# Kernel tuning notes

Measured on AMD Instinct MI355X. Metric: run time of the kernel, lower is better.

## Reference

```python
import jax, jax.numpy as jnp
import numpy as np

B, P, H, A = 256, 196, 1024, 512

def setup_inputs() -> dict:
    key = jax.random.key(0)
    ks = jax.random.split(key, 20)
    s = 1.0 / np.sqrt(H)
    sa = 1.0 / np.sqrt(A)
    return {
        "spatial_image": jax.random.normal(ks[0], (B, P, H), jnp.float32),
        "decoder_out": jax.random.normal(ks[1], (B, H), jnp.float32),
        "st": jax.random.normal(ks[2], (B, H), jnp.float32),
        "W_sen_aff": jax.random.uniform(ks[3], (H, H), jnp.float32, -s, s),
        "b_sen_aff": jax.random.uniform(ks[4], (H,), jnp.float32, -s, s),
        "W_sen_att": jax.random.uniform(ks[5], (H, A), jnp.float32, -s, s),
        "b_sen_att": jax.random.uniform(ks[6], (A,), jnp.float32, -s, s),
        "W_h_aff": jax.random.uniform(ks[7], (H, H), jnp.float32, -s, s),
        "b_h_aff": jax.random.uniform(ks[8], (H,), jnp.float32, -s, s),
        "W_h_att": jax.random.uniform(ks[9], (H, A), jnp.float32, -s, s),
        "b_h_att": jax.random.uniform(ks[10], (A,), jnp.float32, -s, s),
        "W_v_att": jax.random.uniform(ks[11], (H, A), jnp.float32, -s, s),
        "b_v_att": jax.random.uniform(ks[12], (A,), jnp.float32, -s, s),
        "W_alpha": jax.random.uniform(ks[13], (A, 1), jnp.float32, -sa, sa),
        "b_alpha": jax.random.uniform(ks[14], (1,), jnp.float32, -sa, sa),
        "W_ctx": jax.random.uniform(ks[15], (H, H), jnp.float32, -s, s),
        "b_ctx": jax.random.uniform(ks[16], (H,), jnp.float32, -s, s),
    }

def reference(spatial_image, decoder_out, st,
              W_sen_aff, b_sen_aff, W_sen_att, b_sen_att,
              W_h_aff, b_h_aff, W_h_att, b_h_att,
              W_v_att, b_v_att, W_alpha, b_alpha, W_ctx, b_ctx):
    # visual_attn: [B, P, A]
    visual_attn = jnp.einsum('bph,ha->bpa', spatial_image, W_v_att) + b_v_att
    # sentinel path: [B, H] -> relu affine -> [B, A]
    sentinel_affine = jax.nn.relu(st @ W_sen_aff + b_sen_aff)
    sentinel_attn = sentinel_affine @ W_sen_att + b_sen_att
    # hidden path: [B, H] -> tanh affine -> [B, A]
    hidden_affine = jnp.tanh(decoder_out @ W_h_aff + b_h_aff)
    hidden_attn = hidden_affine @ W_h_att + b_h_att
    # concat sentinel as an extra "pixel": [B, P+1, H] and [B, P+1, A]
    concat_features = jnp.concatenate([spatial_image, sentinel_affine[:, None, :]], axis=1)
    attended_features = jnp.concatenate([visual_attn, sentinel_attn[:, None, :]], axis=1)
    attention = jnp.tanh(attended_features + hidden_attn[:, None, :])  # [B, P+1, A]
    alpha = (jnp.einsum('bpa,ao->bpo', attention, W_alpha) + b_alpha)[..., 0]  # [B, P+1]
    att_weights = jax.nn.softmax(alpha, axis=1)
    context = jnp.einsum('bph,bp->bh', concat_features, att_weights)  # [B, H]
    beta_value = att_weights[:, -1:]  # [B, 1]
    out_l = jnp.tanh((context + hidden_affine) @ W_ctx + b_ctx)  # [B, H]
    return (out_l, att_weights, beta_value)
```

## Files before the change

### kernel.cpp

```cpp
#include <hip/hip_runtime.h>
#include <hip/hip_bf16.h>
#include <stdint.h>
#include <stddef.h>

typedef __attribute__((ext_vector_type(4))) float f32x4;
typedef __attribute__((ext_vector_type(8))) short short8;

#define MROWS 50176


static __device__ __forceinline__ int lds_off(int row, int k) {
    int slot = (k >> 3) ^ ((row >> 1) & 3);
    return (row << 6) + (slot << 4) + ((k & 7) << 1);
}

static __device__ __forceinline__ unsigned div196(unsigned g) {
    return (unsigned)(((unsigned long long)g * 85599ull) >> 24);
}

static __device__ __forceinline__ unsigned short f2bf(float f) {
    union { float f; unsigned u; } v; v.f = f;
    unsigned r = v.u + 0x7FFFu + ((v.u >> 16) & 1u);
    return (unsigned short)(r >> 16);
}

static __device__ __forceinline__ unsigned pack2bf(float2 a) {
    union { unsigned u; __hip_bfloat162 h; } r;
    r.h = __float22bfloat162_rn(a);
    return r.u;
}

static __device__ __forceinline__ unsigned long long pack4bf(f32x4 a) {
    union { unsigned long long u; __hip_bfloat162 h[2]; } r;
    r.h[0] = __float22bfloat162_rn(make_float2(a[0], a[1]));
    r.h[1] = __float22bfloat162_rn(make_float2(a[2], a[3]));
    return r.u;
}

static __device__ __forceinline__ float tanh_fast(float x) {
    float xc = fminf(fmaxf(x, -9.f), 9.f);
    float e = __builtin_amdgcn_exp2f(xc * 2.885390081777927f);
    return (e - 1.f) * __builtin_amdgcn_rcpf(e + 1.f);
}

static __device__ __forceinline__ void gload_lds16(const void* g, void* l) {
    __builtin_amdgcn_global_load_lds(
        (const __attribute__((address_space(1))) unsigned int*)g,
        (__attribute__((address_space(3))) unsigned int*)l, 16, 0, 0);
}

__global__ __launch_bounds__(512, 4) void attn_alpha_kernel(
    const float* __restrict__ spatial,
    const unsigned short* __restrict__ WvT,
    const float* __restrict__ b_v_att,
    const float* __restrict__ hidden_attn,
    const float* __restrict__ W_alpha,
    float* __restrict__ alphab)
{
    __shared__ char sA[2][2048];
    __shared__ char sB[32768];
    float* alpha_s = (float*)&sA[0][0];
    const int tid = threadIdx.x;
    const int row0 = blockIdx.x << 5;

    const int lane = tid & 63, w = tid >> 6;
    const int lrow = lane & 15, lk = lane >> 4;

    const int arow = tid >> 4;
    const int acol = (tid & 15) << 1;
    const float* Ap = spatial + (size_t)(row0 + arow) * 1024 + acol;
    const int aoff = lds_off(arow, acol);

    const unsigned short* Bq[4];
    int boff[4];
    #pragma unroll
    for (int c = 0; c < 4; ++c) {
        int row = (c << 7) + (w << 4) + (lane >> 2);
        int ke = (lane & 3) << 3;
        Bq[c] = WvT + (size_t)row * 1024 + ke;
        boff[c] = lds_off(row, ke);
    }

    f32x4 acc[2][4];
    f32x4 z = {0.f, 0.f, 0.f, 0.f};
    #pragma unroll
    for (int m = 0; m < 2; ++m)
        #pragma unroll
        for (int n = 0; n < 4; ++n) acc[m][n] = z;

    {
        float2 a0 = *(const float2*)Ap;
        f32x4 b0[4];
        #pragma unroll
        for (int c = 0; c < 4; ++c) b0[c] = *(const f32x4*)Bq[c];
        *(unsigned*)(sA[0] + aoff) = pack2bf(a0);
        #pragma unroll
        for (int c = 0; c < 4; ++c) *(f32x4*)(sB + boff[c]) = b0[c];
    }
    __syncthreads();

    for (int ks = 0; ks < 32; ++ks) {
        const int cur = ks & 1, nxt = cur ^ 1;
        float2 aN;
        f32x4 bN[4];
        if (ks < 31) {
            const int ko = (ks + 1) << 5;
            aN = *(const float2*)(Ap + ko);
            #pragma unroll
            for (int c = 0; c < 4; ++c) bN[c] = *(const f32x4*)(Bq[c] + ko);
        }
        short8 af[2], bf[4];
        #pragma unroll
        for (int m = 0; m < 2; ++m)
            af[m] = *(const short8*)(sA[cur] + lds_off((m << 4) + lrow, lk << 3));
        #pragma unroll
        for (int n = 0; n < 4; ++n)
            bf[n] = *(const short8*)(sB + lds_off((w << 6) + (n << 4) + lrow, lk << 3));
        #pragma unroll
        for (int m = 0; m < 2; ++m)
            #pragma unroll
            for (int n = 0; n < 4; ++n)
                acc[m][n] = __builtin_amdgcn_mfma_f32_16x16x32_bf16(af[m], bf[n], acc[m][n], 0, 0, 0);
        __syncthreads();
        if (ks < 31) {
            *(unsigned*)(sA[nxt] + aoff) = pack2bf(aN);
            #pragma unroll
            for (int c = 0; c < 4; ++c) *(f32x4*)(sB + boff[c]) = bN[c];
            __syncthreads();
        }
    }

    if (tid < 32) alpha_s[tid] = 0.f;
    __syncthreads();

    const unsigned bb0 = div196((unsigned)row0);
    const unsigned bb1 = div196((unsigned)(row0 + 31));
    float bv[4], wa[4], h0[4], h1[4];
    #pragma unroll
    for (int n = 0; n < 4; ++n) {
        int g = (w << 6) + (n << 4) + lrow;
        bv[n] = b_v_att[g];
        wa[n] = W_alpha[g];
        h0[n] = hidden_attn[bb0 * 512 + g];
        h1[n] = hidden_attn[bb1 * 512 + g];
    }
    #pragma unroll
    for (int m = 0; m < 2; ++m) {
        #pragma unroll
        for (int i = 0; i < 4; ++i) {
            int rloc = (m << 4) + (lk << 2) + i;
            bool first = (div196((unsigned)(row0 + rloc)) == bb0);
            float s = 0.f;
            #pragma unroll
            for (int n = 0; n < 4; ++n) {
                float v = tanh_fast(acc[m][n][i] + bv[n] + (first ? h0[n] : h1[n]));
                s += v * wa[n];
            }
            #pragma unroll
            for (int off = 1; off < 16; off <<= 1) s += __shfl_xor(s, off);
            if (lrow == 0) atomicAdd(&alpha_s[rloc], s);
        }
    }
    __syncthreads();
    if (tid < 32) {
        unsigned g = (unsigned)(row0 + tid);
        unsigned bb = div196(g);
        unsigned p = g - bb * 196;
        alphab[bb * 196 + p] = alpha_s[tid];
    }
}

static __device__ __forceinline__ void kloop_dbuf(
    const float* __restrict__ Abase,
    const unsigned short* __restrict__ Bbase,
    char* sA0, char* sA1, char* sB0, char* sB1,
    f32x4 acc[4][4], int tid)
{
    const int lane = tid & 63, w = tid >> 6;
    const int lrow = lane & 15, lk = lane >> 4;
    const int wr = w >> 1, wc = w & 1;

    const float* Ap[4];
    int aoff[4];
    #pragma unroll
    for (int r = 0; r < 4; ++r) {
        int q = tid + (r << 8);
        int ar = q >> 3, kc = (q & 7) << 2;
        Ap[r] = Abase + (size_t)ar * 1024 + kc;
        aoff[r] = lds_off(ar, kc);
    }
    const unsigned short* Bp[2];
    int bdst[2];
    #pragma unroll
    for (int c = 0; c < 2; ++c) {
        int ch = (w << 1) + c;
        int row = (ch << 4) + (lane >> 2);
        int kg = (lane & 3) ^ ((row >> 1) & 3);
        Bp[c] = Bbase + (size_t)row * 1024 + (kg << 3);
        bdst[c] = ch << 10;
    }

    f32x4 z = {0.f, 0.f, 0.f, 0.f};
    #pragma unroll
    for (int m = 0; m < 4; ++m)
        #pragma unroll
        for (int n = 0; n < 4; ++n) acc[m][n] = z;

    {
        f32x4 a[4];
        #pragma unroll
        for (int r = 0; r < 4; ++r) a[r] = *(const f32x4*)Ap[r];
        #pragma unroll
        for (int c = 0; c < 2; ++c) gload_lds16(Bp[c], sB0 + bdst[c]);
        #pragma unroll
        for (int r = 0; r < 4; ++r)
            *(unsigned long long*)(sA0 + aoff[r]) = pack4bf(a[r]);
    }
    __syncthreads();

    char* sAc = sA0; char* sAn = sA1;
    char* sBc = sB0; char* sBn = sB1;
    for (int ks = 0; ks < 32; ++ks) {
        f32x4 an[4];
        if (ks < 31) {
            const int ko = (ks + 1) << 5;
            #pragma unroll
            for (int r = 0; r < 4; ++r) an[r] = *(const f32x4*)(Ap[r] + ko);
            #pragma unroll
            for (int c = 0; c < 2; ++c) gload_lds16(Bp[c] + ko, sBn + bdst[c]);
        }
        short8 af[4], bf[4];
        #pragma unroll
        for (int m = 0; m < 4; ++m)
            af[m] = *(const short8*)(sAc + lds_off((wr << 6) + (m << 4) + lrow, lk << 3));
        #pragma unroll
        for (int n = 0; n < 4; ++n)
            bf[n] = *(const short8*)(sBc + lds_off((wc << 6) + (n << 4) + lrow, lk << 3));
        #pragma unroll
        for (int m = 0; m < 4; ++m)
            #pragma unroll
            for (int n = 0; n < 4; ++n)
                acc[m][n] = __builtin_amdgcn_mfma_f32_16x16x32_bf16(af[m], bf[n], acc[m][n], 0, 0, 0);
        if (ks < 31) {
            #pragma unroll
            for (int r = 0; r < 4; ++r)
                *(unsigned long long*)(sAn + aoff[r]) = pack4bf(an[r]);
        }
        __syncthreads();
        char* t;
        t = sAc; sAc = sAn; sAn = t;
        t = sBc; sBc = sBn; sBn = t;
    }
}

struct GemmDesc { const float* A; const unsigned short* BT; const float* bias; float* C; int N; int act; };
struct GemmPair { GemmDesc d[2]; };

__global__ __launch_bounds__(256, 4) void gemm_pair_kernel(GemmPair p)
{
    GemmDesc d = p.d[blockIdx.z];
    __shared__ char sA[2][8192];
    __shared__ char sB[2][8192];
    const int tid = threadIdx.x;
    const int row0 = blockIdx.x << 7;
    const int col0 = blockIdx.y << 7;
    f32x4 acc[4][4];
    kloop_dbuf(d.A + (size_t)row0 * 1024, d.BT + (size_t)col0 * 1024,
               sA[0], sA[1], sB[0], sB[1], acc, tid);
    const int lane = tid & 63, w = tid >> 6;
    const int wr = w >> 1, wc = w & 1;
    const int lrow = lane & 15, lk = lane >> 4;
    #pragma unroll
    for (int n = 0; n < 4; ++n) {
        int col = col0 + (wc << 6) + (n << 4) + lrow;
        float bs = d.bias[col];
        #pragma unroll
        for (int m = 0; m < 4; ++m) {
            int rbase = row0 + (wr << 6) + (m << 4) + (lk << 2);
            #pragma unroll
            for (int i = 0; i < 4; ++i) {
                float v = acc[m][n][i] + bs;
                if (d.act == 1) v = fmaxf(v, 0.f);
                if (d.act == 2) v = tanh_fast(v);
                d.C[(size_t)(rbase + i) * d.N + col] = v;
            }
        }
    }
}

struct TransDesc { const float* src; unsigned short* dst; int K; int N; };
struct TransArgs { TransDesc d[6]; };

__global__ void transpose_cvt_kernel(TransArgs args) {
    TransDesc d = args.d[blockIdx.y];
    int nt = d.N >> 5;
    int tiles = (d.K >> 5) * nt;
    if ((int)blockIdx.x >= tiles) return;
    int tk = blockIdx.x / nt, tn = blockIdx.x % nt;
    __shared__ unsigned short tile[32][33];
    int tx = threadIdx.x & 31, ty = threadIdx.x >> 5;
    int k0 = tk << 5, n0 = tn << 5;
    #pragma unroll
    for (int j = 0; j < 4; ++j)
        tile[ty + j * 8][tx] = f2bf(d.src[(size_t)(k0 + ty + j * 8) * d.N + n0 + tx]);
    __syncthreads();
    #pragma unroll
    for (int j = 0; j < 4; ++j)
        d.dst[(size_t)(n0 + ty + j * 8) * d.K + k0 + tx] = tile[tx][ty + j * 8];
}

__global__ void softmax_sentinel_kernel(
    const float* __restrict__ alphab,
    const float* __restrict__ sen_att, const float* __restrict__ hid_att,
    const float* __restrict__ W_alpha,
    float* __restrict__ att, float* __restrict__ beta)
{
    int b = blockIdx.x, tid = threadIdx.x;
    __shared__ float al[197];
    __shared__ float red[4];
    if (tid < 196) al[tid] = alphab[b * 196 + tid];
    float s = 0.f;
    for (int a = tid; a < 512; a += 256)
        s += tanh_fast(sen_att[b * 512 + a] + hid_att[b * 512 + a]) * W_alpha[a];
    #pragma unroll
    for (int off = 1; off < 64; off <<= 1) s += __shfl_xor(s, off);
    if ((tid & 63) == 0) red[tid >> 6] = s;
    __syncthreads();
    if (tid == 0) al[196] = red[0] + red[1] + red[2] + red[3];
    __syncthreads();
    if (tid < 64) {
        float v[4];
        float mx = -1e30f;
        #pragma unroll
        for (int jj = 0; jj < 4; ++jj) {
            int i = tid + jj * 64;
            v[jj] = (i < 197) ? al[i] : -1e30f;
            mx = fmaxf(mx, v[jj]);
        }
        #pragma unroll
        for (int off = 1; off < 64; off <<= 1) mx = fmaxf(mx, __shfl_xor(mx, off));
        float sm = 0.f;
        #pragma unroll
        for (int jj = 0; jj < 4; ++jj) {
            v[jj] = __builtin_amdgcn_exp2f((v[jj] - mx) * 1.442695040888963f);
            if (tid + jj * 64 >= 197) v[jj] = 0.f;
            sm += v[jj];
        }
        #pragma unroll
        for (int off = 1; off < 64; off <<= 1) sm += __shfl_xor(sm, off);
        float inv = 1.f / sm;
        #pragma unroll
        for (int jj = 0; jj < 4; ++jj) {
            int i = tid + jj * 64;
            if (i < 197) {
                float wv = v[jj] * inv;
                att[b * 197 + i] = wv;
                if (i == 196) beta[b] = wv;
            }
        }
    }
}

__global__ __launch_bounds__(256) void context_kernel(
    const float* __restrict__ spatial, const float* __restrict__ sen_aff,
    const float* __restrict__ hid_aff, const float* __restrict__ att,
    float* __restrict__ ctxh)
{
    int b = blockIdx.x, half = blockIdx.y, t = threadIdx.x;
    __shared__ float wsm[197];
    if (t < 197) wsm[t] = att[b * 197 + t];
    __syncthreads();
    int h2 = (half << 8) + t;
    const float2* sp = (const float2*)(spatial + (size_t)b * 196 * 1024) + h2;
    float ax = 0.f, ay = 0.f;
    #pragma unroll 8
    for (int p = 0; p < 196; ++p) {
        float2 x = sp[(size_t)p * 512];
        ax += wsm[p] * x.x; ay += wsm[p] * x.y;
    }
    float w196 = wsm[196];
    float2 sa = ((const float2*)(sen_aff + (size_t)b * 1024))[h2];
    float2 ha = ((const float2*)(hid_aff + (size_t)b * 1024))[h2];
    ctxh[(size_t)b * 1024 + 2 * h2]     = ax + w196 * sa.x + ha.x;
    ctxh[(size_t)b * 1024 + 2 * h2 + 1] = ay + w196 * sa.y + ha.y;
}

extern "C" void kernel_launch(void* const* d_in, const int* in_sizes, int n_in,
                              void* d_out, int out_size, void* d_ws, size_t ws_size,
                              hipStream_t stream)
{
    const float* spatial   = (const float*)d_in[0];
    const float* decoder   = (const float*)d_in[1];
    const float* st        = (const float*)d_in[2];
    const float* W_sen_aff = (const float*)d_in[3];
    const float* b_sen_aff = (const float*)d_in[4];
    const float* W_sen_att = (const float*)d_in[5];
    const float* b_sen_att = (const float*)d_in[6];
    const float* W_h_aff   = (const float*)d_in[7];
    const float* b_h_aff   = (const float*)d_in[8];
    const float* W_h_att   = (const float*)d_in[9];
    const float* b_h_att   = (const float*)d_in[10];
    const float* W_v_att   = (const float*)d_in[11];
    const float* b_v_att   = (const float*)d_in[12];
    const float* W_alpha   = (const float*)d_in[13];
    const float* W_ctx     = (const float*)d_in[15];
    const float* b_ctx     = (const float*)d_in[16];

    char* ws = (char*)d_ws;
    size_t off = 0;
    auto alloc = [&](size_t bytes) {
        char* p = ws + off; off += (bytes + 255) & ~(size_t)255; return p;
    };
    unsigned short* WvT  = (unsigned short*)alloc((size_t)512 * 1024 * 2);
    unsigned short* WsaT = (unsigned short*)alloc((size_t)1024 * 1024 * 2);
    unsigned short* WstT = (unsigned short*)alloc((size_t)512 * 1024 * 2);
    unsigned short* WhaT = (unsigned short*)alloc((size_t)1024 * 1024 * 2);
    unsigned short* WhtT = (unsigned short*)alloc((size_t)512 * 1024 * 2);
    unsigned short* WcxT = (unsigned short*)alloc((size_t)1024 * 1024 * 2);
    float* sen_aff = (float*)alloc((size_t)256 * 1024 * 4);
    float* sen_att = (float*)alloc((size_t)256 * 512 * 4);
    float* hid_aff = (float*)alloc((size_t)256 * 1024 * 4);
    float* hid_att = (float*)alloc((size_t)256 * 512 * 4);
    float* alphab  = (float*)alloc((size_t)MROWS * 4);
    float* ctxh    = (float*)alloc((size_t)256 * 1024 * 4);

    float* out_l    = (float*)d_out;
    float* out_att  = out_l + 256 * 1024;
    float* out_beta = out_att + 256 * 197;

    TransArgs ta;
    ta.d[0] = { W_v_att,   WvT,  1024, 512  };
    ta.d[1] = { W_sen_aff, WsaT, 1024, 1024 };
    ta.d[2] = { W_sen_att, WstT, 1024, 512  };
    ta.d[3] = { W_h_aff,   WhaT, 1024, 1024 };
    ta.d[4] = { W_h_att,   WhtT, 1024, 512  };
    ta.d[5] = { W_ctx,     WcxT, 1024, 1024 };
    transpose_cvt_kernel<<<dim3(1024, 6), 256, 0, stream>>>(ta);

    GemmPair p1;
    p1.d[0] = { st,      WsaT, b_sen_aff, sen_aff, 1024, 1 };
    p1.d[1] = { decoder, WhaT, b_h_aff,   hid_aff, 1024, 2 };
    gemm_pair_kernel<<<dim3(2, 8, 2), 256, 0, stream>>>(p1);

    GemmPair p2;
    p2.d[0] = { sen_aff, WstT, b_sen_att, sen_att, 512, 0 };
    p2.d[1] = { hid_aff, WhtT, b_h_att,   hid_att, 512, 0 };
    gemm_pair_kernel<<<dim3(2, 4, 2), 256, 0, stream>>>(p2);

    attn_alpha_kernel<<<1568, 512, 0, stream>>>(spatial, WvT, b_v_att, hid_att, W_alpha, alphab);
    softmax_sentinel_kernel<<<256, 256, 0, stream>>>(alphab, sen_att, hid_att, W_alpha, out_att, out_beta);
    context_kernel<<<dim3(256, 2), 256, 0, stream>>>(spatial, sen_aff, hid_aff, out_att, ctxh);

    GemmPair p3;
    p3.d[0] = { ctxh, WcxT, b_ctx, out_l, 1024, 2 };
    p3.d[1] = { ctxh, WcxT, b_ctx, out_l, 1024, 2 };
    gemm_pair_kernel<<<dim3(2, 8, 1), 256, 0, stream>>>(p3);
}
```

Before: 259.4 us.

## Stage full A tile in LDS once and stream B fragments directly from global

The attention-alpha GEMM now converts the block's whole 32x1024 slice of spatial features to bf16 into a 64KB swizzled LDS buffer up front. B (transposed W_v_att) fragments are then read straight from global/L2 into registers each k-step, with no per-step LDS staging or barriers. Blocks shrink to 256 threads, each wave covering 128 output columns (8 MFMA tiles per row group). This removes the double-buffer synchronisation in the k-loop, but it adds more register pressure, depends on L2 latency for B loads, and the large LDS footprint limits occupancy.

```diff
diff --git a/kernel.cpp b/kernel.cpp
--- a/kernel.cpp
+++ b/kernel.cpp
@@ -22,12 +22,6 @@
     union { float f; unsigned u; } v; v.f = f;
     unsigned r = v.u + 0x7FFFu + ((v.u >> 16) & 1u);
     return (unsigned short)(r >> 16);
-}
-
-static __device__ __forceinline__ unsigned pack2bf(float2 a) {
-    union { unsigned u; __hip_bfloat162 h; } r;
-    r.h = __float22bfloat162_rn(a);
-    return r.u;
 }
 
 static __device__ __forceinline__ unsigned long long pack4bf(f32x4 a) {
@@ -37,6 +31,15 @@
     return r.u;
 }
 
+static __device__ __forceinline__ short8 cvt8bf(f32x4 lo, f32x4 hi) {
+    union { short8 s; __hip_bfloat162 h[4]; } u;
+    u.h[0] = __float22bfloat162_rn(make_float2(lo[0], lo[1]));
+    u.h[1] = __float22bfloat162_rn(make_float2(lo[2], lo[3]));
+    u.h[2] = __float22bfloat162_rn(make_float2(hi[0], hi[1]));
+    u.h[3] = __float22bfloat162_rn(make_float2(hi[2], hi[3]));
+    return u.s;
+}
+
 static __device__ __forceinline__ float tanh_fast(float x) {
     float xc = fminf(fmaxf(x, -9.f), 9.f);
     float e = __builtin_amdgcn_exp2f(xc * 2.885390081777927f);
@@ -49,7 +52,7 @@
         (__attribute__((address_space(3))) unsigned int*)l, 16, 0, 0);
 }
 
-__global__ __launch_bounds__(512, 4) void attn_alpha_kernel(
+__global__ __launch_bounds__(256, 2) void attn_alpha_kernel(
     const float* __restrict__ spatial,
     const unsigned short* __restrict__ WvT,
     const float* __restrict__ b_v_att,
@@ -57,88 +60,76 @@
     const float* __restrict__ W_alpha,
     float* __restrict__ alphab)
 {
-    __shared__ char sA[2][2048];
-    __shared__ char sB[32768];
-    float* alpha_s = (float*)&sA[0][0];
+    __shared__ char sA[65536];
+    float* alpha_s = (float*)sA;
     const int tid = threadIdx.x;
     const int row0 = blockIdx.x << 5;
 
     const int lane = tid & 63, w = tid >> 6;
     const int lrow = lane & 15, lk = lane >> 4;
 
-    const int arow = tid >> 4;
-    const int acol = (tid & 15) << 1;
-    const float* Ap = spatial + (size_t)(row0 + arow) * 1024 + acol;
-    const int aoff = lds_off(arow, acol);
-
-    const unsigned short* Bq[4];
-    int boff[4];
-    #pragma unroll
-    for (int c = 0; c < 4; ++c) {
-        int row = (c << 7) + (w << 4) + (lane >> 2);
-        int ke = (lane & 3) << 3;
-        Bq[c] = WvT + (size_t)row * 1024 + ke;
-        boff[c] = lds_off(row, ke);
-    }
-
-    f32x4 acc[2][4];
+    {
+        const int ar = tid >> 3;
+        const int cb = (tid & 7) << 3;
+        const float* Arow = spatial + (size_t)(row0 + ar) * 1024 + cb;
+        char* Lrow = sA + (ar << 11);
+        const int rx = ar & 7;
+        #pragma unroll 4
+        for (int j = 0; j < 16; ++j) {
+            f32x4 lo = *(const f32x4*)(Arow + (j << 6));
+            f32x4 hi = *(const f32x4*)(Arow + (j << 6) + 4);
+            int s = (cb >> 3) + (j << 3);
+            *(short8*)(Lrow + ((s ^ rx) << 4)) = cvt8bf(lo, hi);
+        }
+    }
+    __syncthreads();
+
+    const unsigned short* Bp[8];
+    #pragma unroll
+    for (int n = 0; n < 8; ++n)
+        Bp[n] = WvT + (size_t)((w << 7) + (n << 4) + lrow) * 1024 + (lk << 3);
+
+    const int rx = lrow & 7;
+    int abase[2];
+    #pragma unroll
+    for (int m = 0; m < 2; ++m) abase[m] = ((m << 4) + lrow) << 11;
+
+    f32x4 acc[2][8];
     f32x4 z = {0.f, 0.f, 0.f, 0.f};
     #pragma unroll
     for (int m = 0; m < 2; ++m)
         #pragma unroll
-        for (int n = 0; n < 4; ++n) acc[m][n] = z;
-
-    {
-        float2 a0 = *(const float2*)Ap;
-        f32x4 b0[4];
-        #pragma unroll
-        for (int c = 0; c < 4; ++c) b0[c] = *(const f32x4*)Bq[c];
-        *(unsigned*)(sA[0] + aoff) = pack2bf(a0);
-        #pragma unroll
-        for (int c = 0; c < 4; ++c) *(f32x4*)(sB + boff[c]) = b0[c];
-    }
-    __syncthreads();
-
+        for (int n = 0; n < 8; ++n) acc[m][n] = z;
+
+    #pragma unroll 4
     for (int ks = 0; ks < 32; ++ks) {
-        const int cur = ks & 1, nxt = cur ^ 1;
-        float2 aN;
-        f32x4 bN[4];
-        if (ks < 31) {
-            const int ko = (ks + 1) << 5;
-            aN = *(const float2*)(Ap + ko);
-            #pragma unroll
-            for (int c = 0; c < 4; ++c) bN[c] = *(const f32x4*)(Bq[c] + ko);
-        }
-        short8 af[2], bf[4];
+        short8 bf[8];
+        #pragma unroll
+        for (int n = 0; n < 8; ++n)
+            bf[n] = *(const short8*)(Bp[n] + (ks << 5));
+        short8 af[2];
+        #pragma unroll
+        for (int m = 0; m < 2; ++m) {
+            int slot = ((ks << 2) + lk) ^ rx;
+            af[m] = *(const short8*)(sA + abase[m] + (slot << 4));
+        }
         #pragma unroll
         for (int m = 0; m < 2; ++m)
-            af[m] = *(const short8*)(sA[cur] + lds_off((m << 4) + lrow, lk << 3));
-        #pragma unroll
-        for (int n = 0; n < 4; ++n)
-            bf[n] = *(const short8*)(sB + lds_off((w << 6) + (n << 4) + lrow, lk << 3));
-        #pragma unroll
-        for (int m = 0; m < 2; ++m)
-            #pragma unroll
-            for (int n = 0; n < 4; ++n)
+            #pragma unroll
+            for (int n = 0; n < 8; ++n)
                 acc[m][n] = __builtin_amdgcn_mfma_f32_16x16x32_bf16(af[m], bf[n], acc[m][n], 0, 0, 0);
-        __syncthreads();
-        if (ks < 31) {
-            *(unsigned*)(sA[nxt] + aoff) = pack2bf(aN);
-            #pragma unroll
-            for (int c = 0; c < 4; ++c) *(f32x4*)(sB + boff[c]) = bN[c];
-            __syncthreads();
-        }
-    }
-
+    }
+
+    __syncthreads();
     if (tid < 32) alpha_s[tid] = 0.f;
     __syncthreads();
 
     const unsigned bb0 = div196((unsigned)row0);
     const unsigned bb1 = div196((unsigned)(row0 + 31));
-    float bv[4], wa[4], h0[4], h1[4];
-    #pragma unroll
-    for (int n = 0; n < 4; ++n) {
-        int g = (w << 6) + (n << 4) + lrow;
+    float bv[8], wa[8], h0[8], h1[8];
+    #pragma unroll
+    for (int n = 0; n < 8; ++n) {
+        int g = (w << 7) + (n << 4) + lrow;
         bv[n] = b_v_att[g];
         wa[n] = W_alpha[g];
         h0[n] = hidden_attn[bb0 * 512 + g];
@@ -152,7 +143,7 @@
             bool first = (div196((unsigned)(row0 + rloc)) == bb0);
             float s = 0.f;
             #pragma unroll
-            for (int n = 0; n < 4; ++n) {
+            for (int n = 0; n < 8; ++n) {
                 float v = tanh_fast(acc[m][n][i] + bv[n] + (first ? h0[n] : h1[n]));
                 s += v * wa[n];
             }
@@ -447,7 +438,7 @@
     p2.d[1] = { hid_aff, WhtT, b_h_att,   hid_att, 512, 0 };
     gemm_pair_kernel<<<dim3(2, 4, 2), 256, 0, stream>>>(p2);
 
-    attn_alpha_kernel<<<1568, 512, 0, stream>>>(spatial, WvT, b_v_att, hid_att, W_alpha, alphab);
+    attn_alpha_kernel<<<1568, 256, 0, stream>>>(spatial, WvT, b_v_att, hid_att, W_alpha, alphab);
     softmax_sentinel_kernel<<<256, 256, 0, stream>>>(alphab, sen_att, hid_att, W_alpha, out_att, out_beta);
     context_kernel<<<dim3(256, 2), 256, 0, stream>>>(spatial, sen_aff, hid_aff, out_att, ctxh);
 
```

Result: slower. 340.7 us (+31.3%).
